# Optimization experiments

Measured on AMD Instinct MI355X. Metric: run time of the kernel, lower is better.

The kernel has to match this reference:

```python
import jax, jax.numpy as jnp
import numpy as np


def layer_norm(x, w, b, eps=1e-5):
    mu = jnp.mean(x, axis=-1, keepdims=True)
    var = jnp.mean(jnp.square(x - mu), axis=-1, keepdims=True)
    return (x - mu) / jnp.sqrt(var + eps) * w + b


def setup_inputs() -> dict:
    B, T, S, D, K = 8, 2048, 2048, 512, 3
    ks = jax.random.split(jax.random.key(0), 8)
    w_scale = 0.02  # modest init so softmax/layernorm stay in a sane range
    return {
        "x": jax.random.normal(ks[0], (B, T, D), jnp.float32),
        "enc": jax.random.normal(ks[1], (B, S, D), jnp.float32),
        "conv_w": jax.random.normal(ks[2], (2 * D, D, K), jnp.float32) * w_scale,
        "conv_b": jnp.zeros((2 * D,), jnp.float32),
        "ln1_w": jnp.ones((D,), jnp.float32),
        "ln1_b": jnp.zeros((D,), jnp.float32),
        "Wq": jax.random.normal(ks[3], (D, D), jnp.float32) * w_scale,
        "bq": jnp.zeros((D,), jnp.float32),
        "Wk": jax.random.normal(ks[4], (D, D), jnp.float32) * w_scale,
        "bk": jnp.zeros((D,), jnp.float32),
        "Wv": jax.random.normal(ks[5], (D, D), jnp.float32) * w_scale,
        "bv": jnp.zeros((D,), jnp.float32),
        "Wo": jax.random.normal(ks[6], (D, D), jnp.float32) * w_scale,
        "bo": jnp.zeros((D,), jnp.float32),
        "ln2_w": jnp.ones((D,), jnp.float32),
        "ln2_b": jnp.zeros((D,), jnp.float32),
    }


def reference(x, enc, conv_w, conv_b, ln1_w, ln1_b, Wq, bq, Wk, bk, Wv, bv, Wo, bo, ln2_w, ln2_b):
    D = x.shape[-1]
    K = conv_w.shape[-1]
    # Causal GLU: left-pad by K-1 so each output sees only past/current positions.
    xt = jnp.transpose(x, (0, 2, 1))  # [B, D, T]
    xt = jnp.pad(xt, ((0, 0), (0, 0), (K - 1, 0)))
    conv = jax.lax.conv_general_dilated(
        xt, conv_w, window_strides=(1,), padding="VALID",
        dimension_numbers=("NCH", "OIH", "NCH"))
    conv = conv + conv_b[None, :, None]
    conv = jnp.transpose(conv, (0, 2, 1))  # [B, T, 2D]
    a, g = jnp.split(conv, 2, axis=-1)
    glu = a * jax.nn.sigmoid(g)
    # residual + LN1 (dropout is identity in eval mode)
    h = layer_norm(glu + x, ln1_w, ln1_b)
    # cross-attention: bmm -> softmax -> bmm (single head)
    q = h @ Wq.T + bq            # [B, T, D]
    k = enc @ Wk.T + bk          # [B, S, D]
    v = enc @ Wv.T + bv          # [B, S, D]
    scores = jnp.einsum("btd,bsd->bts", q, k) / jnp.sqrt(jnp.float32(D))
    attn = jax.nn.softmax(scores, axis=-1)  # [B, T, S]
    ctx = jnp.einsum("bts,bsd->btd", attn, v)
    ctx = ctx @ Wo.T + bo
    out = layer_norm(h + ctx, ln2_w, ln2_b)
    return out, attn
```

## Files before the change

### kernel.cpp

```cpp
#include <hip/hip_runtime.h>
#include <hip/hip_bf16.h>
#include <stdint.h>


typedef unsigned short ushortT;
typedef __bf16 bf16x8 __attribute__((ext_vector_type(8)));
typedef float floatx4 __attribute__((ext_vector_type(4)));
typedef unsigned short ushort4v __attribute__((ext_vector_type(4)));
typedef unsigned short ushort8 __attribute__((ext_vector_type(8)));

__device__ __forceinline__ ushortT f2bf(float f) {
  unsigned u = __builtin_bit_cast(unsigned, f);
  u += 0x7FFFu + ((u >> 16) & 1u);
  return (ushortT)(u >> 16);
}
__device__ __forceinline__ float bf2f(ushortT u) {
  return __builtin_bit_cast(float, (unsigned)u << 16);
}

__device__ __forceinline__ void gload_lds16(const void* g, void* l) {
  __builtin_amdgcn_global_load_lds(
      (const __attribute__((address_space(1))) void*)g,
      (__attribute__((address_space(3))) void*)l, 16, 0, 0);
}

__global__ __launch_bounds__(256)
void k_f32_to_bf16v(const float* __restrict__ src, ushortT* __restrict__ dst, long n4) {
  long i = (long)blockIdx.x * 256 + threadIdx.x;
  if (i >= n4) return;
  floatx4 v = *(const floatx4*)&src[i * 4];
  ushort4v o;
#pragma unroll
  for (int j = 0; j < 4; j++) o[j] = f2bf(v[j]);
  *(ushort4v*)&dst[i * 4] = o;
}

__global__ __launch_bounds__(256)
void k_w4(const float* __restrict__ w0, const float* __restrict__ w1,
          const float* __restrict__ w2, const float* __restrict__ w3,
          ushortT* __restrict__ dst) {
  long i = (long)blockIdx.x * 256 + threadIdx.x;
  int m = (int)(i >> 16);
  long within = (i & 65535) * 4;
  const float* s = (m == 0) ? w0 : (m == 1) ? w1 : (m == 2) ? w2 : w3;
  floatx4 v = *(const floatx4*)&s[within];
  ushort4v o;
#pragma unroll
  for (int j = 0; j < 4; j++) o[j] = f2bf(v[j]);
  *(ushort4v*)&dst[(long)m * 262144 + within] = o;
}

__global__ __launch_bounds__(128)
void k_xpad(const float* __restrict__ x, ushortT* __restrict__ xp) {
  int row = blockIdx.x;
  int b = row / 2050, tp = row % 2050;
  int c = threadIdx.x * 4;
  ushort4v o = {0, 0, 0, 0};
  if (tp >= 2) {
    floatx4 v = *(const floatx4*)&x[((long)(b * 2048 + tp - 2)) * 512 + c];
#pragma unroll
    for (int j = 0; j < 4; j++) o[j] = f2bf(v[j]);
  }
  *(ushort4v*)&xp[(long)row * 512 + c] = o;
}

__global__ __launch_bounds__(256)
void k_convw(const float* __restrict__ w, ushortT* __restrict__ dst) {
  long idx = (long)blockIdx.x * 256 + threadIdx.x;
  if (idx >= 1024L * 1536) return;
  int n = (int)(idx / 1536), kk = (int)(idx % 1536);
  int tap = kk >> 9, i = kk & 511;
  int o = ((n >> 4) & 1) * 512 + (n >> 5) * 16 + (n & 15);
  dst[idx] = f2bf(w[(o * 512 + i) * 3 + tap]);
}

template<int CONV_A, int GLU, int BIAS, int WBF16, int DUALZ, int SWAP>
__global__ __launch_bounds__(512)
void k_gemm256(const ushortT* __restrict__ A, const ushortT* __restrict__ A2, int lda, long aBatch,
               const ushortT* __restrict__ Bm, const ushortT* __restrict__ Bm2, int ldb, long bBatch,
               const float* __restrict__ bias, const float* __restrict__ bias2,
               const float* __restrict__ xres,
               float* __restrict__ Cf, ushortT* __restrict__ Cb, ushortT* __restrict__ Cb2,
               long cBatch, int ldc, int Kdim, float scale)
{
  __shared__ ushortT lds[2][2 * 16384];

  const int tid  = threadIdx.x;
  const int lane = tid & 63;
  const int wave = tid >> 6;
  const int wr   = wave >> 2;
  const int wc   = wave & 3;
  const int l15  = lane & 15;
  const int quad = lane >> 4;

  const ushortT* Ap = A;
  const ushortT* Bp = Bm;
  const float* biasP = bias;
  ushortT* CbP = Cb;
  if (DUALZ && blockIdx.z) { Ap = A2; Bp = Bm2; biasP = bias2; CbP = Cb2; }
  const long zA = DUALZ ? 0 : (long)blockIdx.z * aBatch;
  const long zB = DUALZ ? 0 : (long)blockIdx.z * bBatch;
  const long zC = DUALZ ? 0 : (long)blockIdx.z * cBatch;
  const int rowBase = (SWAP ? blockIdx.y : blockIdx.x) * 256;
  const int colBase = (SWAP ? blockIdx.x : blockIdx.y) * 256;

  auto STAGE = [&](int t) {
    ushortT* sA = lds[t & 1];
    ushortT* sB = sA + 16384;
    const int k0 = t << 6;
#pragma unroll
    for (int l = 0; l < 4; l++) {
      int idx = l * 512 + tid;
      int row = idx >> 3;
      int ck  = ((tid & 7) ^ (row & 7)) << 3;
      if (CONV_A) {
        int gr = rowBase + row;
        int gc = k0 + ck;
        int tap = gc >> 9, ii = gc & 511;
        int b = gr >> 11, tt = gr & 2047;
        long gofs = ((long)(b * 2050 + tt + tap) << 9) + ii;
        gload_lds16(Ap + gofs, sA + idx * 8);
      } else {
        long gofs = zA + (long)(rowBase + row) * lda + (k0 + ck);
        gload_lds16(Ap + gofs, sA + idx * 8);
      }
    }
#pragma unroll
    for (int l = 0; l < 4; l++) {
      int idx = l * 512 + tid;
      int row = idx >> 3;
      int ck  = ((tid & 7) ^ (row & 7)) << 3;
      long gofs = zB + (long)(colBase + row) * ldb + (k0 + ck);
      gload_lds16(Bp + gofs, sB + idx * 8);
    }
  };

  auto LD = [&](const ushortT* s, int r, int c) -> bf16x8 {
    return *(const bf16x8*)&s[r * 64 + ((c ^ (r & 7)) << 3)];
  };

  floatx4 zero = {0.f, 0.f, 0.f, 0.f};
  floatx4 acc[8][4];
#pragma unroll
  for (int mi = 0; mi < 8; mi++)
#pragma unroll
    for (int ni = 0; ni < 4; ni++) acc[mi][ni] = zero;

  const int NT = Kdim >> 6;
  STAGE(0);
  STAGE(1);

  for (int t = 0; t < NT; t++) {
    if (t < NT - 1) asm volatile("s_waitcnt vmcnt(8)" ::: "memory");
    else            asm volatile("s_waitcnt vmcnt(0)" ::: "memory");
    __builtin_amdgcn_s_barrier();

    const ushortT* sA = lds[t & 1];
    const ushortT* sB = sA + 16384;

    bf16x8 av[4][2], bv[4][2];
#pragma unroll
    for (int ni = 0; ni < 4; ni++)
#pragma unroll
      for (int ks = 0; ks < 2; ks++)
        bv[ni][ks] = LD(sB, wc * 64 + ni * 16 + l15, ks * 4 + quad);
#pragma unroll
    for (int mi = 0; mi < 4; mi++)
#pragma unroll
      for (int ks = 0; ks < 2; ks++)
        av[mi][ks] = LD(sA, wr * 128 + mi * 16 + l15, ks * 4 + quad);

    __builtin_amdgcn_s_setprio(1);
#pragma unroll
    for (int mi = 0; mi < 4; mi++)
#pragma unroll
      for (int ni = 0; ni < 4; ni++)
#pragma unroll
        for (int ks = 0; ks < 2; ks++)
          acc[mi][ni] = __builtin_amdgcn_mfma_f32_16x16x32_bf16(av[mi][ks], bv[ni][ks], acc[mi][ni], 0, 0, 0);
    __builtin_amdgcn_s_setprio(0);

#pragma unroll
    for (int mi = 0; mi < 4; mi++)
#pragma unroll
      for (int ks = 0; ks < 2; ks++)
        av[mi][ks] = LD(sA, wr * 128 + 64 + mi * 16 + l15, ks * 4 + quad);

    __builtin_amdgcn_s_setprio(1);
#pragma unroll
    for (int mi = 0; mi < 4; mi++)
#pragma unroll
      for (int ni = 0; ni < 4; ni++)
#pragma unroll
        for (int ks = 0; ks < 2; ks++)
          acc[4 + mi][ni] = __builtin_amdgcn_mfma_f32_16x16x32_bf16(av[mi][ks], bv[ni][ks], acc[4 + mi][ni], 0, 0, 0);
    __builtin_amdgcn_s_setprio(0);

    __builtin_amdgcn_s_barrier();
    if (t + 2 < NT) STAGE(t + 2);
  }

  if (GLU) {
#pragma unroll
    for (int mi = 0; mi < 8; mi++) {
#pragma unroll
      for (int ni = 0; ni < 4; ni += 2) {
        int colA = colBase + wc * 64 + ni * 16;
        int d = (colA >> 5) * 16 + l15;
        float ba = biasP[d], bg = biasP[512 + d];
#pragma unroll
        for (int r = 0; r < 4; r++) {
          int grow = rowBase + wr * 128 + mi * 16 + quad * 4 + r;
          float a = acc[mi][ni][r] + ba;
          float g = acc[mi][ni + 1][r] + bg;
          float val = a / (1.0f + __expf(-g)) + xres[(long)grow * 512 + d];
          Cf[(long)grow * 512 + d] = val;
        }
      }
    }
  } else {
#pragma unroll
    for (int mi = 0; mi < 8; mi++) {
#pragma unroll
      for (int ni = 0; ni < 4; ni++) {
        int gcol = colBase + wc * 64 + ni * 16 + l15;
        float bcol = BIAS ? biasP[gcol] : 0.0f;
#pragma unroll
        for (int r = 0; r < 4; r++) {
          int grow = rowBase + wr * 128 + mi * 16 + quad * 4 + r;
          float val = acc[mi][ni][r] * scale + bcol;
          long off = zC + (long)grow * ldc + gcol;
          if (WBF16) CbP[off] = f2bf(val);
          else       Cf[off] = val;
        }
      }
    }
  }
}

template<int BIAS, int WBF16, int LNEPI>
__global__ __launch_bounds__(512)
void k_gemm64(const ushortT* __restrict__ A, int lda, long aBatch,
              const ushortT* __restrict__ Bm, int ldb, long bBatch,
              const float* __restrict__ bias, const ushortT* __restrict__ hres,
              const float* __restrict__ lnw, const float* __restrict__ lnb,
              float* __restrict__ Cf, ushortT* __restrict__ Cb,
              long cBatch, int ldc, int Kdim, float scale)
{
  __shared__ ushortT lds[2][(64 + 512) * 64];

  const int tid  = threadIdx.x;
  const int lane = tid & 63;
  const int wave = tid >> 6;
  const int l15  = lane & 15;
  const int quad = lane >> 4;

  const long zA = (long)blockIdx.z * aBatch;
  const long zB = (long)blockIdx.z * bBatch;
  const long zC = (long)blockIdx.z * cBatch;
  const int rowBase = blockIdx.y * 64;
  const int colBase = blockIdx.x * 512;

  auto STAGE = [&](int t) {
    ushortT* sA = lds[t & 1];
    ushortT* sB = sA + 64 * 64;
    const int k0 = t << 6;
    {
      int row = tid >> 3;
      int ck  = ((tid & 7) ^ (row & 7)) << 3;
      long gofs = zA + (long)(rowBase + row) * lda + (k0 + ck);
      gload_lds16(A + gofs, sA + tid * 8);
    }
#pragma unroll
    for (int l = 0; l < 8; l++) {
      int idx = l * 512 + tid;
      int row = idx >> 3;
      int ck  = ((tid & 7) ^ (row & 7)) << 3;
      long gofs = zB + (long)(colBase + row) * ldb + (k0 + ck);
      gload_lds16(Bm + gofs, sB + idx * 8);
    }
  };

  auto LD = [&](const ushortT* s, int r, int c) -> bf16x8 {
    return *(const bf16x8*)&s[r * 64 + ((c ^ (r & 7)) << 3)];
  };

  floatx4 zero = {0.f, 0.f, 0.f, 0.f};
  floatx4 acc[4][4];
#pragma unroll
  for (int mi = 0; mi < 4; mi++)
#pragma unroll
    for (int ni = 0; ni < 4; ni++) acc[mi][ni] = zero;

  const int NT = Kdim >> 6;
  STAGE(0);
  STAGE(1);

  for (int t = 0; t < NT; t++) {
    if (t < NT - 1) asm volatile("s_waitcnt vmcnt(9)" ::: "memory");
    else            asm volatile("s_waitcnt vmcnt(0)" ::: "memory");
    __builtin_amdgcn_s_barrier();

    const ushortT* sA = lds[t & 1];
    const ushortT* sB = sA + 64 * 64;

    bf16x8 av[4][2], bv[4][2];
#pragma unroll
    for (int ni = 0; ni < 4; ni++)
#pragma unroll
      for (int ks = 0; ks < 2; ks++)
        bv[ni][ks] = LD(sB, wave * 64 + ni * 16 + l15, ks * 4 + quad);
#pragma unroll
    for (int mi = 0; mi < 4; mi++)
#pragma unroll
      for (int ks = 0; ks < 2; ks++)
        av[mi][ks] = LD(sA, mi * 16 + l15, ks * 4 + quad);

    __builtin_amdgcn_s_setprio(1);
#pragma unroll
    for (int mi = 0; mi < 4; mi++)
#pragma unroll
      for (int ni = 0; ni < 4; ni++)
#pragma unroll
        for (int ks = 0; ks < 2; ks++)
          acc[mi][ni] = __builtin_amdgcn_mfma_f32_16x16x32_bf16(av[mi][ks], bv[ni][ks], acc[mi][ni], 0, 0, 0);
    __builtin_amdgcn_s_setprio(0);

    __builtin_amdgcn_s_barrier();
    if (t + 2 < NT) STAGE(t + 2);
  }

  if (LNEPI) {
    float bov[4], lw[4], lb[4];
#pragma unroll
    for (int ni = 0; ni < 4; ni++) {
      int col = wave * 64 + ni * 16 + l15;
      bov[ni] = bias[col]; lw[ni] = lnw[col]; lb[ni] = lnb[col];
    }
    float* psum = (float*)&lds[0][0];
    float* pssq = psum + 8 * 64;
    __syncthreads();
#pragma unroll
    for (int mi = 0; mi < 4; mi++) {
#pragma unroll
      for (int r = 0; r < 4; r++) {
        int rowl = mi * 16 + quad * 4 + r;
        long grow = rowBase + rowl;
        float ps = 0.f, pq = 0.f;
#pragma unroll
        for (int ni = 0; ni < 4; ni++) {
          int col = wave * 64 + ni * 16 + l15;
          float val = acc[mi][ni][r] + bov[ni] + bf2f(hres[grow * 512 + col]);
          acc[mi][ni][r] = val;
          ps += val; pq += val * val;
        }
#pragma unroll
        for (int off = 1; off < 16; off <<= 1) { ps += __shfl_xor(ps, off); pq += __shfl_xor(pq, off); }
        if (l15 == 0) { psum[wave * 64 + rowl] = ps; pssq[wave * 64 + rowl] = pq; }
      }
    }
    __syncthreads();
#pragma unroll
    for (int mi = 0; mi < 4; mi++) {
#pragma unroll
      for (int r = 0; r < 4; r++) {
        int rowl = mi * 16 + quad * 4 + r;
        float S = 0.f, Q = 0.f;
#pragma unroll
        for (int w = 0; w < 8; w++) { S += psum[w * 64 + rowl]; Q += pssq[w * 64 + rowl]; }
        float mu = S * (1.0f / 512.0f);
        float rstd = rsqrtf(Q * (1.0f / 512.0f) - mu * mu + 1e-5f);
        long grow = rowBase + rowl;
#pragma unroll
        for (int ni = 0; ni < 4; ni++) {
          int col = wave * 64 + ni * 16 + l15;
          Cf[grow * 512 + col] = (acc[mi][ni][r] - mu) * rstd * lw[ni] + lb[ni];
        }
      }
    }
  } else {
#pragma unroll
    for (int mi = 0; mi < 4; mi++) {
#pragma unroll
      for (int ni = 0; ni < 4; ni++) {
        int gcol = colBase + wave * 64 + ni * 16 + l15;
        float bcol = (BIAS == 1) ? bias[gcol] : 0.0f;
#pragma unroll
        for (int r = 0; r < 4; r++) {
          int grow = rowBase + mi * 16 + quad * 4 + r;
          float val = acc[mi][ni][r] * scale + bcol + ((BIAS == 2) ? bias[grow] : 0.0f);
          long off = zC + (long)grow * ldc + gcol;
          if (WBF16) Cb[off] = f2bf(val);
          else       Cf[off] = val;
        }
      }
    }
  }
}

__global__ __launch_bounds__(128)
void k_ln(const float* __restrict__ src, const float* __restrict__ w, const float* __restrict__ b,
          ushortT* __restrict__ outb)
{
  __shared__ float s1[2], s2[2];
  long r = blockIdx.x;
  int tid = threadIdx.x;
  floatx4 v = *(const floatx4*)&src[r * 512 + tid * 4];
  float sum = v[0] + v[1] + v[2] + v[3];
  float ssq = v[0]*v[0] + v[1]*v[1] + v[2]*v[2] + v[3]*v[3];
#pragma unroll
  for (int off = 32; off; off >>= 1) { sum += __shfl_xor(sum, off); ssq += __shfl_xor(ssq, off); }
  if ((tid & 63) == 0) { s1[tid >> 6] = sum; s2[tid >> 6] = ssq; }
  __syncthreads();
  sum = s1[0] + s1[1]; ssq = s2[0] + s2[1];
  float mu = sum * (1.0f / 512.0f);
  float var = ssq * (1.0f / 512.0f) - mu * mu;
  float rstd = rsqrtf(var + 1e-5f);
  floatx4 wv = *(const floatx4*)&w[tid * 4];
  floatx4 bv = *(const floatx4*)&b[tid * 4];
  ushort4v ob;
#pragma unroll
  for (int j = 0; j < 4; j++) ob[j] = f2bf((v[j] - mu) * rstd * wv[j] + bv[j]);
  *(ushort4v*)&outb[r * 512 + tid * 4] = ob;
}

__global__ __launch_bounds__(256)
void k_softmax(ushortT* __restrict__ logits, float* __restrict__ attn)
{
  __shared__ float sred[4];
  long r = blockIdx.x;
  ushortT* lrow = logits + r * 2048;
  float* arow = attn + r * 2048;
  int tid = threadIdx.x;
  ushort8 uv = *(const ushort8*)&lrow[tid * 8];
  float v[8];
#pragma unroll
  for (int j = 0; j < 8; j++) v[j] = bf2f(uv[j]);
  float mx = v[0];
#pragma unroll
  for (int j = 1; j < 8; j++) mx = fmaxf(mx, v[j]);
#pragma unroll
  for (int off = 32; off; off >>= 1) mx = fmaxf(mx, __shfl_xor(mx, off));
  if ((tid & 63) == 0) sred[tid >> 6] = mx;
  __syncthreads();
  mx = fmaxf(fmaxf(sred[0], sred[1]), fmaxf(sred[2], sred[3]));
  __syncthreads();
  float sum = 0.f;
#pragma unroll
  for (int j = 0; j < 8; j++) { v[j] = __expf(v[j] - mx); sum += v[j]; }
#pragma unroll
  for (int off = 32; off; off >>= 1) sum += __shfl_xor(sum, off);
  if ((tid & 63) == 0) sred[tid >> 6] = sum;
  __syncthreads();
  sum = sred[0] + sred[1] + sred[2] + sred[3];
  float inv = 1.0f / sum;
  floatx4 o0, o1;
  ushort8 ob;
#pragma unroll
  for (int j = 0; j < 8; j++) {
    float p = v[j] * inv;
    if (j < 4) o0[j] = p; else o1[j - 4] = p;
    ob[j] = f2bf(p);
  }
  *(floatx4*)&arow[tid * 8] = o0;
  *(floatx4*)&arow[tid * 8 + 4] = o1;
  *(ushort8*)&lrow[tid * 8] = ob;
}

extern "C" void kernel_launch(void* const* d_in, const int* in_sizes, int n_in,
                              void* d_out, int out_size, void* d_ws, size_t ws_size,
                              hipStream_t stream)
{
  const float* x      = (const float*)d_in[0];
  const float* enc    = (const float*)d_in[1];
  const float* conv_w = (const float*)d_in[2];
  const float* conv_b = (const float*)d_in[3];
  const float* ln1_w  = (const float*)d_in[4];
  const float* ln1_b  = (const float*)d_in[5];
  const float* Wq     = (const float*)d_in[6];
  const float* bq     = (const float*)d_in[7];
  const float* Wk     = (const float*)d_in[8];
  const float* bk     = (const float*)d_in[9];
  const float* Wv     = (const float*)d_in[10];
  const float* bv     = (const float*)d_in[11];
  const float* Wo     = (const float*)d_in[12];
  const float* bo     = (const float*)d_in[13];
  const float* ln2_w  = (const float*)d_in[14];
  const float* ln2_b  = (const float*)d_in[15];

  const long BT = 16384, Dd = 512, S = 2048, TT = 2048;
  float* out  = (float*)d_out;
  float* attn = out + BT * Dd;

  char* p = (char*)d_ws;
  auto alloc = [&](size_t bytes) { char* r = p; p += (bytes + 255) & ~255UL; return r; };
  float*   hglu  = (float*)alloc(BT * Dd * 4);
  ushortT* xpad  = (ushortT*)alloc(8L * 2050 * 512 * 2);
  ushortT* encbf = (ushortT*)alloc(BT * Dd * 2);
  ushortT* hbf   = (ushortT*)alloc(BT * Dd * 2);
  ushortT* qbf   = (ushortT*)alloc(BT * Dd * 2);
  ushortT* kbf   = (ushortT*)alloc(BT * Dd * 2);
  ushortT* vT    = (ushortT*)alloc(Dd * BT * 2);
  ushortT* ctxbf = (ushortT*)alloc(BT * Dd * 2);
  ushortT* sl    = (ushortT*)alloc(BT * S * 2);
  ushortT* Wcbf  = (ushortT*)alloc(1024L * 1536 * 2);
  ushortT* wall  = (ushortT*)alloc(4L * 262144 * 2);
  ushortT* Wqbf = wall, *Wkbf = wall + 262144, *Wvbf = wall + 2 * 262144, *Wobf = wall + 3 * 262144;

  k_xpad<<<8 * 2050, 128, 0, stream>>>(x, xpad);
  k_f32_to_bf16v<<<(BT * Dd / 4 + 255) / 256, 256, 0, stream>>>(enc, encbf, BT * Dd / 4);
  k_convw<<<(1024 * 1536 + 255) / 256, 256, 0, stream>>>(conv_w, Wcbf);
  k_w4<<<1024, 256, 0, stream>>>(Wq, Wk, Wv, Wo, wall);

  k_gemm256<1, 1, 0, 0, 0, 0><<<dim3(64, 4, 1), 512, 0, stream>>>(
      xpad, nullptr, 0, 0, Wcbf, nullptr, 1536, 0,
      conv_b, nullptr, x, hglu, nullptr, nullptr, 0, 512, 1536, 1.0f);
  k_ln<<<16384, 128, 0, stream>>>(hglu, ln1_w, ln1_b, hbf);

  k_gemm256<0, 0, 1, 1, 1, 0><<<dim3(64, 2, 2), 512, 0, stream>>>(
      hbf, encbf, 512, 0, Wqbf, Wkbf, 512, 0,
      bq, bk, nullptr, nullptr, qbf, kbf, 0, 512, 512, 1.0f);

  k_gemm64<2, 1, 0><<<dim3(32, 8, 1), 512, 0, stream>>>(
      Wvbf, 512, 0, encbf, 512, 0,
      bv, nullptr, nullptr, nullptr,
      nullptr, vT, 0, 16384, 512, 1.0f);

  k_gemm256<0, 0, 0, 1, 0, 0><<<dim3(8, 8, 8), 512, 0, stream>>>(
      qbf, nullptr, 512, TT * Dd, kbf, nullptr, 512, S * Dd,
      nullptr, nullptr, nullptr, nullptr, sl, nullptr,
      TT * S, 2048, 512, 0.04419417382415922f);
  k_softmax<<<16384, 256, 0, stream>>>(sl, attn);

  k_gemm64<0, 1, 0><<<dim3(1, 32, 8), 512, 0, stream>>>(
      sl, 2048, TT * S, vT, 16384, TT,
      nullptr, nullptr, nullptr, nullptr,
      nullptr, ctxbf, TT * Dd, 512, 2048, 1.0f);

  k_gemm64<0, 0, 1><<<dim3(1, 256, 1), 512, 0, stream>>>(
      ctxbf, 512, 0, Wobf, 512, 0,
      bo, hbf, ln2_w, ln2_b,
      out, nullptr, 0, 512, 512, 1.0f);
}
```

Measured before the change: 531.2 us.

## Fuse softmax into attention-context GEMM and interleave 256-tile GEMM staging loads

Removes the standalone softmax kernel. A new kernel first computes each row's max and sum from the bf16 logits, then normalizes the probabilities on the fly while staging them into LDS for the P·V GEMM, writing the fp32 attn output along the way. This drops a full read-modify-write pass over the bf16 logits and one launch. The logits are now read twice for the row statistics plus once more for the GEMM. Separately, the 256-tile GEMM splits its prefetch into B and A halves and issues them between the two MFMA phases, with an extra barrier, to overlap loads with compute.

```diff
diff --git a/kernel.cpp b/kernel.cpp
--- a/kernel.cpp
+++ b/kernel.cpp
@@ -104,35 +104,32 @@
   const int rowBase = (SWAP ? blockIdx.y : blockIdx.x) * 256;
   const int colBase = (SWAP ? blockIdx.x : blockIdx.y) * 256;
 
-  auto STAGE = [&](int t) {
+  auto STAGE_A = [&](int t, int l) {
     ushortT* sA = lds[t & 1];
-    ushortT* sB = sA + 16384;
     const int k0 = t << 6;
-#pragma unroll
-    for (int l = 0; l < 4; l++) {
-      int idx = l * 512 + tid;
-      int row = idx >> 3;
-      int ck  = ((tid & 7) ^ (row & 7)) << 3;
-      if (CONV_A) {
-        int gr = rowBase + row;
-        int gc = k0 + ck;
-        int tap = gc >> 9, ii = gc & 511;
-        int b = gr >> 11, tt = gr & 2047;
-        long gofs = ((long)(b * 2050 + tt + tap) << 9) + ii;
-        gload_lds16(Ap + gofs, sA + idx * 8);
-      } else {
-        long gofs = zA + (long)(rowBase + row) * lda + (k0 + ck);
-        gload_lds16(Ap + gofs, sA + idx * 8);
-      }
-    }
-#pragma unroll
-    for (int l = 0; l < 4; l++) {
-      int idx = l * 512 + tid;
-      int row = idx >> 3;
-      int ck  = ((tid & 7) ^ (row & 7)) << 3;
-      long gofs = zB + (long)(colBase + row) * ldb + (k0 + ck);
-      gload_lds16(Bp + gofs, sB + idx * 8);
-    }
+    int idx = l * 512 + tid;
+    int row = idx >> 3;
+    int ck  = ((tid & 7) ^ (row & 7)) << 3;
+    if (CONV_A) {
+      int gr = rowBase + row;
+      int gc = k0 + ck;
+      int tap = gc >> 9, ii = gc & 511;
+      int b = gr >> 11, tt = gr & 2047;
+      long gofs = ((long)(b * 2050 + tt + tap) << 9) + ii;
+      gload_lds16(Ap + gofs, sA + idx * 8);
+    } else {
+      long gofs = zA + (long)(rowBase + row) * lda + (k0 + ck);
+      gload_lds16(Ap + gofs, sA + idx * 8);
+    }
+  };
+  auto STAGE_B = [&](int t, int l) {
+    ushortT* sB = lds[t & 1] + 16384;
+    const int k0 = t << 6;
+    int idx = l * 512 + tid;
+    int row = idx >> 3;
+    int ck  = ((tid & 7) ^ (row & 7)) << 3;
+    long gofs = zB + (long)(colBase + row) * ldb + (k0 + ck);
+    gload_lds16(Bp + gofs, sB + idx * 8);
   };
 
   auto LD = [&](const ushortT* s, int r, int c) -> bf16x8 {
@@ -147,8 +144,14 @@
     for (int ni = 0; ni < 4; ni++) acc[mi][ni] = zero;
 
   const int NT = Kdim >> 6;
-  STAGE(0);
-  STAGE(1);
+#pragma unroll
+  for (int l = 0; l < 4; l++) { STAGE_B(0, l); }
+#pragma unroll
+  for (int l = 0; l < 4; l++) { STAGE_A(0, l); }
+#pragma unroll
+  for (int l = 0; l < 4; l++) { STAGE_B(1, l); }
+#pragma unroll
+  for (int l = 0; l < 4; l++) { STAGE_A(1, l); }
 
   for (int t = 0; t < NT; t++) {
     if (t < NT - 1) asm volatile("s_waitcnt vmcnt(8)" ::: "memory");
@@ -180,11 +183,18 @@
           acc[mi][ni] = __builtin_amdgcn_mfma_f32_16x16x32_bf16(av[mi][ks], bv[ni][ks], acc[mi][ni], 0, 0, 0);
     __builtin_amdgcn_s_setprio(0);
 
+    __builtin_amdgcn_s_barrier();
+
 #pragma unroll
     for (int mi = 0; mi < 4; mi++)
 #pragma unroll
       for (int ks = 0; ks < 2; ks++)
         av[mi][ks] = LD(sA, wr * 128 + 64 + mi * 16 + l15, ks * 4 + quad);
+
+    if (t + 2 < NT) {
+      STAGE_B(t + 2, 0); STAGE_B(t + 2, 1); STAGE_B(t + 2, 2); STAGE_B(t + 2, 3);
+      STAGE_A(t + 2, 0); STAGE_A(t + 2, 2);
+    }
 
     __builtin_amdgcn_s_setprio(1);
 #pragma unroll
@@ -197,7 +207,7 @@
     __builtin_amdgcn_s_setprio(0);
 
     __builtin_amdgcn_s_barrier();
-    if (t + 2 < NT) STAGE(t + 2);
+    if (t + 2 < NT) { STAGE_A(t + 2, 1); STAGE_A(t + 2, 3); }
   }
 
   if (GLU) {
@@ -398,6 +408,150 @@
   }
 }
 
+__global__ __launch_bounds__(512)
+void k_ctx_sm(const ushortT* __restrict__ logit,
+              const ushortT* __restrict__ vT,
+              float* __restrict__ attn,
+              ushortT* __restrict__ ctxb)
+{
+  __shared__ ushortT sB[2][512 * 64];
+  __shared__ ushortT sA[2][64 * 64];
+  __shared__ float rowM[64], rowInv[64];
+
+  const int tid = threadIdx.x, lane = tid & 63, wave = tid >> 6;
+  const int l15 = lane & 15, quad = lane >> 4;
+  const int z = blockIdx.z;
+  const int rowBase = blockIdx.y * 64;
+  const long lrowBase = (long)z * 2048 + rowBase;
+
+  {
+    int r = tid >> 3, c0 = (tid & 7) * 256;
+    const ushortT* lp = logit + (lrowBase + r) * 2048 + c0;
+    float m = -3.0e38f;
+    for (int i = 0; i < 32; i++) {
+      ushort8 u = *(const ushort8*)&lp[i * 8];
+#pragma unroll
+      for (int j = 0; j < 8; j++) m = fmaxf(m, bf2f(u[j]));
+    }
+    m = fmaxf(m, __shfl_xor(m, 1));
+    m = fmaxf(m, __shfl_xor(m, 2));
+    m = fmaxf(m, __shfl_xor(m, 4));
+    float s = 0.f;
+    for (int i = 0; i < 32; i++) {
+      ushort8 u = *(const ushort8*)&lp[i * 8];
+#pragma unroll
+      for (int j = 0; j < 8; j++) s += __expf(bf2f(u[j]) - m);
+    }
+    s += __shfl_xor(s, 1);
+    s += __shfl_xor(s, 2);
+    s += __shfl_xor(s, 4);
+    if ((tid & 7) == 0) { rowM[r] = m; rowInv[r] = 1.0f / s; }
+  }
+  __syncthreads();
+
+  const int rA = tid >> 3, cA = tid & 7;
+  const float Mr = rowM[rA], Ir = rowInv[rA];
+
+  auto STAGEB = [&](int t) {
+    ushortT* d = sB[t & 1];
+    const int k0 = t << 6;
+#pragma unroll
+    for (int l = 0; l < 8; l++) {
+      int idx = l * 512 + tid;
+      int row = idx >> 3;
+      int ck = ((tid & 7) ^ (row & 7)) << 3;
+      long gofs = (long)row * 16384 + (long)z * 2048 + k0 + ck;
+      gload_lds16(vT + gofs, d + idx * 8);
+    }
+  };
+  auto ALOAD = [&](int t) -> ushort8 {
+    return *(const ushort8*)&logit[(lrowBase + rA) * 2048 + (t << 6) + cA * 8];
+  };
+  auto APUT = [&](int t, ushort8 u) {
+    floatx4 p0, p1;
+    ushort8 pb;
+#pragma unroll
+    for (int j = 0; j < 8; j++) {
+      float p = __expf(bf2f(u[j]) - Mr) * Ir;
+      if (j < 4) p0[j] = p; else p1[j - 4] = p;
+      pb[j] = f2bf(p);
+    }
+    float* ap = attn + (lrowBase + rA) * 2048 + (t << 6) + cA * 8;
+    *(floatx4*)ap = p0;
+    *(floatx4*)(ap + 4) = p1;
+    *(ushort8*)&sA[t & 1][rA * 64 + ((cA ^ (rA & 7)) << 3)] = pb;
+  };
+  auto LD = [&](const ushortT* s, int r, int c) -> bf16x8 {
+    return *(const bf16x8*)&s[r * 64 + ((c ^ (r & 7)) << 3)];
+  };
+
+  floatx4 zero = {0.f, 0.f, 0.f, 0.f};
+  floatx4 acc[4][4];
+#pragma unroll
+  for (int mi = 0; mi < 4; mi++)
+#pragma unroll
+    for (int ni = 0; ni < 4; ni++) acc[mi][ni] = zero;
+
+  const int NT = 32;
+  ushort8 aCur = ALOAD(0); STAGEB(0);
+  ushort8 aNxt = ALOAD(1); STAGEB(1);
+  APUT(0, aCur);
+  asm volatile("s_waitcnt vmcnt(9)" ::: "memory");
+  asm volatile("s_waitcnt lgkmcnt(0)" ::: "memory");
+  __builtin_amdgcn_s_barrier();
+
+  ushort8 aNew = aNxt;
+  for (int t = 0; t < NT; t++) {
+    const ushortT* cA_ = sA[t & 1];
+    const ushortT* cB_ = sB[t & 1];
+    bf16x8 av[4][2], bv[4][2];
+#pragma unroll
+    for (int ni = 0; ni < 4; ni++)
+#pragma unroll
+      for (int ks = 0; ks < 2; ks++)
+        bv[ni][ks] = LD(cB_, wave * 64 + ni * 16 + l15, ks * 4 + quad);
+#pragma unroll
+    for (int mi = 0; mi < 4; mi++)
+#pragma unroll
+      for (int ks = 0; ks < 2; ks++)
+        av[mi][ks] = LD(cA_, mi * 16 + l15, ks * 4 + quad);
+
+    __builtin_amdgcn_s_setprio(1);
+#pragma unroll
+    for (int mi = 0; mi < 4; mi++)
+#pragma unroll
+      for (int ni = 0; ni < 4; ni++)
+#pragma unroll
+        for (int ks = 0; ks < 2; ks++)
+          acc[mi][ni] = __builtin_amdgcn_mfma_f32_16x16x32_bf16(av[mi][ks], bv[ni][ks], acc[mi][ni], 0, 0, 0);
+    __builtin_amdgcn_s_setprio(0);
+
+    __builtin_amdgcn_s_barrier();
+    if (t + 2 < NT) { aNew = ALOAD(t + 2); STAGEB(t + 2); }
+    if (t + 1 < NT) {
+      if (t + 2 < NT) asm volatile("s_waitcnt vmcnt(9)" ::: "memory");
+      else            asm volatile("s_waitcnt vmcnt(0)" ::: "memory");
+      APUT(t + 1, aNxt);
+      aNxt = aNew;
+      asm volatile("s_waitcnt lgkmcnt(0)" ::: "memory");
+    }
+    __builtin_amdgcn_s_barrier();
+  }
+
+#pragma unroll
+  for (int mi = 0; mi < 4; mi++) {
+#pragma unroll
+    for (int ni = 0; ni < 4; ni++) {
+      int col = wave * 64 + ni * 16 + l15;
+#pragma unroll
+      for (int r = 0; r < 4; r++) {
+        long grow = lrowBase + mi * 16 + quad * 4 + r;
+        ctxb[grow * 512 + col] = f2bf(acc[mi][ni][r]);
+      }
+    }
+  }
+}
+
 __global__ __launch_bounds__(128)
 void k_ln(const float* __restrict__ src, const float* __restrict__ w, const float* __restrict__ b,
           ushortT* __restrict__ outb)
@@ -422,49 +576,6 @@
 #pragma unroll
   for (int j = 0; j < 4; j++) ob[j] = f2bf((v[j] - mu) * rstd * wv[j] + bv[j]);
   *(ushort4v*)&outb[r * 512 + tid * 4] = ob;
-}
-
-__global__ __launch_bounds__(256)
-void k_softmax(ushortT* __restrict__ logits, float* __restrict__ attn)
-{
-  __shared__ float sred[4];
-  long r = blockIdx.x;
-  ushortT* lrow = logits + r * 2048;
-  float* arow = attn + r * 2048;
-  int tid = threadIdx.x;
-  ushort8 uv = *(const ushort8*)&lrow[tid * 8];
-  float v[8];
-#pragma unroll
-  for (int j = 0; j < 8; j++) v[j] = bf2f(uv[j]);
-  float mx = v[0];
-#pragma unroll
-  for (int j = 1; j < 8; j++) mx = fmaxf(mx, v[j]);
-#pragma unroll
-  for (int off = 32; off; off >>= 1) mx = fmaxf(mx, __shfl_xor(mx, off));
-  if ((tid & 63) == 0) sred[tid >> 6] = mx;
-  __syncthreads();
-  mx = fmaxf(fmaxf(sred[0], sred[1]), fmaxf(sred[2], sred[3]));
-  __syncthreads();
-  float sum = 0.f;
-#pragma unroll
-  for (int j = 0; j < 8; j++) { v[j] = __expf(v[j] - mx); sum += v[j]; }
-#pragma unroll
-  for (int off = 32; off; off >>= 1) sum += __shfl_xor(sum, off);
-  if ((tid & 63) == 0) sred[tid >> 6] = sum;
-  __syncthreads();
-  sum = sred[0] + sred[1] + sred[2] + sred[3];
-  float inv = 1.0f / sum;
-  floatx4 o0, o1;
-  ushort8 ob;
-#pragma unroll
-  for (int j = 0; j < 8; j++) {
-    float p = v[j] * inv;
-    if (j < 4) o0[j] = p; else o1[j - 4] = p;
-    ob[j] = f2bf(p);
-  }
-  *(floatx4*)&arow[tid * 8] = o0;
-  *(floatx4*)&arow[tid * 8 + 4] = o1;
-  *(ushort8*)&lrow[tid * 8] = ob;
 }
 
 extern "C" void kernel_launch(void* const* d_in, const int* in_sizes, int n_in,
@@ -530,12 +641,8 @@
       qbf, nullptr, 512, TT * Dd, kbf, nullptr, 512, S * Dd,
       nullptr, nullptr, nullptr, nullptr, sl, nullptr,
       TT * S, 2048, 512, 0.04419417382415922f);
-  k_softmax<<<16384, 256, 0, stream>>>(sl, attn);
-
-  k_gemm64<0, 1, 0><<<dim3(1, 32, 8), 512, 0, stream>>>(
-      sl, 2048, TT * S, vT, 16384, TT,
-      nullptr, nullptr, nullptr, nullptr,
-      nullptr, ctxbf, TT * Dd, 512, 2048, 1.0f);
+
+  k_ctx_sm<<<dim3(1, 32, 8), 512, 0, stream>>>(sl, vT, attn, ctxbf);
 
   k_gemm64<0, 0, 1><<<dim3(1, 256, 1), 512, 0, stream>>>(
       ctxbf, 512, 0, Wobf, 512, 0,
```

Result: no change. 538.9 us (+1.5%).

## Interleave next-tile loads into GEMM compute and retile the attention-context GEMM

Applied to the files above, without the earlier changes.

The 256x256 GEMM now splits tile staging into per-slice A and B loads. Part of the next-next tile's loads (all of B and half of A) is issued between the two MFMA halves, once an extra barrier guarantees the overwritten LDS regions are no longer being read. This overlaps global-to-LDS traffic with matrix-core work instead of bunching it at the end of the iteration. The attn·V product also moves from the generic 64-row kernel to a dedicated 128x256-tile kernel with batch-interleaved block indices, which changes per-block reuse and the work split. The trade-offs are an extra barrier per iteration and a fragile ordering between LDS reads and async writes into the same buffer.

```diff
diff --git a/kernel.cpp b/kernel.cpp
--- a/kernel.cpp
+++ b/kernel.cpp
@@ -104,35 +104,32 @@
   const int rowBase = (SWAP ? blockIdx.y : blockIdx.x) * 256;
   const int colBase = (SWAP ? blockIdx.x : blockIdx.y) * 256;
 
-  auto STAGE = [&](int t) {
+  auto STAGE_A = [&](int t, int l) {
     ushortT* sA = lds[t & 1];
-    ushortT* sB = sA + 16384;
     const int k0 = t << 6;
-#pragma unroll
-    for (int l = 0; l < 4; l++) {
-      int idx = l * 512 + tid;
-      int row = idx >> 3;
-      int ck  = ((tid & 7) ^ (row & 7)) << 3;
-      if (CONV_A) {
-        int gr = rowBase + row;
-        int gc = k0 + ck;
-        int tap = gc >> 9, ii = gc & 511;
-        int b = gr >> 11, tt = gr & 2047;
-        long gofs = ((long)(b * 2050 + tt + tap) << 9) + ii;
-        gload_lds16(Ap + gofs, sA + idx * 8);
-      } else {
-        long gofs = zA + (long)(rowBase + row) * lda + (k0 + ck);
-        gload_lds16(Ap + gofs, sA + idx * 8);
-      }
-    }
-#pragma unroll
-    for (int l = 0; l < 4; l++) {
-      int idx = l * 512 + tid;
-      int row = idx >> 3;
-      int ck  = ((tid & 7) ^ (row & 7)) << 3;
-      long gofs = zB + (long)(colBase + row) * ldb + (k0 + ck);
-      gload_lds16(Bp + gofs, sB + idx * 8);
-    }
+    int idx = l * 512 + tid;
+    int row = idx >> 3;
+    int ck  = ((tid & 7) ^ (row & 7)) << 3;
+    if (CONV_A) {
+      int gr = rowBase + row;
+      int gc = k0 + ck;
+      int tap = gc >> 9, ii = gc & 511;
+      int b = gr >> 11, tt = gr & 2047;
+      long gofs = ((long)(b * 2050 + tt + tap) << 9) + ii;
+      gload_lds16(Ap + gofs, sA + idx * 8);
+    } else {
+      long gofs = zA + (long)(rowBase + row) * lda + (k0 + ck);
+      gload_lds16(Ap + gofs, sA + idx * 8);
+    }
+  };
+  auto STAGE_B = [&](int t, int l) {
+    ushortT* sB = lds[t & 1] + 16384;
+    const int k0 = t << 6;
+    int idx = l * 512 + tid;
+    int row = idx >> 3;
+    int ck  = ((tid & 7) ^ (row & 7)) << 3;
+    long gofs = zB + (long)(colBase + row) * ldb + (k0 + ck);
+    gload_lds16(Bp + gofs, sB + idx * 8);
   };
 
   auto LD = [&](const ushortT* s, int r, int c) -> bf16x8 {
@@ -147,8 +144,14 @@
     for (int ni = 0; ni < 4; ni++) acc[mi][ni] = zero;
 
   const int NT = Kdim >> 6;
-  STAGE(0);
-  STAGE(1);
+#pragma unroll
+  for (int l = 0; l < 4; l++) { STAGE_B(0, l); }
+#pragma unroll
+  for (int l = 0; l < 4; l++) { STAGE_A(0, l); }
+#pragma unroll
+  for (int l = 0; l < 4; l++) { STAGE_B(1, l); }
+#pragma unroll
+  for (int l = 0; l < 4; l++) { STAGE_A(1, l); }
 
   for (int t = 0; t < NT; t++) {
     if (t < NT - 1) asm volatile("s_waitcnt vmcnt(8)" ::: "memory");
@@ -180,11 +183,18 @@
           acc[mi][ni] = __builtin_amdgcn_mfma_f32_16x16x32_bf16(av[mi][ks], bv[ni][ks], acc[mi][ni], 0, 0, 0);
     __builtin_amdgcn_s_setprio(0);
 
+    __builtin_amdgcn_s_barrier();
+
 #pragma unroll
     for (int mi = 0; mi < 4; mi++)
 #pragma unroll
       for (int ks = 0; ks < 2; ks++)
         av[mi][ks] = LD(sA, wr * 128 + 64 + mi * 16 + l15, ks * 4 + quad);
+
+    if (t + 2 < NT) {
+      STAGE_B(t + 2, 0); STAGE_B(t + 2, 1); STAGE_B(t + 2, 2); STAGE_B(t + 2, 3);
+      STAGE_A(t + 2, 0); STAGE_A(t + 2, 2);
+    }
 
     __builtin_amdgcn_s_setprio(1);
 #pragma unroll
@@ -197,7 +207,7 @@
     __builtin_amdgcn_s_setprio(0);
 
     __builtin_amdgcn_s_barrier();
-    if (t + 2 < NT) STAGE(t + 2);
+    if (t + 2 < NT) { STAGE_A(t + 2, 1); STAGE_A(t + 2, 3); }
   }
 
   if (GLU) {
@@ -233,6 +243,113 @@
           if (WBF16) CbP[off] = f2bf(val);
           else       Cf[off] = val;
         }
+      }
+    }
+  }
+}
+
+__global__ __launch_bounds__(512)
+void k_ctx128(const ushortT* __restrict__ P,
+              const ushortT* __restrict__ vT,
+              ushortT* __restrict__ ctxb)
+{
+  __shared__ ushortT lds[2][(128 + 256) * 64];
+
+  const int tid  = threadIdx.x;
+  const int lane = tid & 63;
+  const int wave = tid >> 6;
+  const int wr   = wave >> 2;
+  const int wc   = wave & 3;
+  const int l15  = lane & 15;
+  const int quad = lane >> 4;
+
+  const int lid = blockIdx.x;
+  const int z   = lid & 7;
+  const int idx = lid >> 3;
+  const int rowBase = (idx >> 1) * 128;
+  const int colBase = (idx & 1) * 256;
+  const long zA = (long)z * 2048 * 2048;
+
+  auto STAGE = [&](int t) {
+    ushortT* sA = lds[t & 1];
+    ushortT* sB = sA + 128 * 64;
+    const int k0 = t << 6;
+#pragma unroll
+    for (int l = 0; l < 2; l++) {
+      int i2 = l * 512 + tid;
+      int row = i2 >> 3;
+      int ck  = ((tid & 7) ^ (row & 7)) << 3;
+      long gofs = zA + (long)(rowBase + row) * 2048 + (k0 + ck);
+      gload_lds16(P + gofs, sA + i2 * 8);
+    }
+#pragma unroll
+    for (int l = 0; l < 4; l++) {
+      int i2 = l * 512 + tid;
+      int row = i2 >> 3;
+      int ck  = ((tid & 7) ^ (row & 7)) << 3;
+      long gofs = (long)(colBase + row) * 16384 + (long)z * 2048 + (k0 + ck);
+      gload_lds16(vT + gofs, sB + i2 * 8);
+    }
+  };
+
+  auto LD = [&](const ushortT* s, int r, int c) -> bf16x8 {
+    return *(const bf16x8*)&s[r * 64 + ((c ^ (r & 7)) << 3)];
+  };
+
+  floatx4 zero = {0.f, 0.f, 0.f, 0.f};
+  floatx4 acc[4][4];
+#pragma unroll
+  for (int mi = 0; mi < 4; mi++)
+#pragma unroll
+    for (int ni = 0; ni < 4; ni++) acc[mi][ni] = zero;
+
+  const int NT = 32;
+  STAGE(0);
+  STAGE(1);
+
+  for (int t = 0; t < NT; t++) {
+    if (t < NT - 1) asm volatile("s_waitcnt vmcnt(6)" ::: "memory");
+    else            asm volatile("s_waitcnt vmcnt(0)" ::: "memory");
+    __builtin_amdgcn_s_barrier();
+
+    const ushortT* sA = lds[t & 1];
+    const ushortT* sB = sA + 128 * 64;
+
+    bf16x8 av[4][2], bv[4][2];
+#pragma unroll
+    for (int ni = 0; ni < 4; ni++)
+#pragma unroll
+      for (int ks = 0; ks < 2; ks++)
+        bv[ni][ks] = LD(sB, wc * 64 + ni * 16 + l15, ks * 4 + quad);
+#pragma unroll
+    for (int mi = 0; mi < 4; mi++)
+#pragma unroll
+      for (int ks = 0; ks < 2; ks++)
+        av[mi][ks] = LD(sA, wr * 64 + mi * 16 + l15, ks * 4 + quad);
+
+    __builtin_amdgcn_s_setprio(1);
+#pragma unroll
+    for (int mi = 0; mi < 4; mi++)
+#pragma unroll
+      for (int ni = 0; ni < 4; ni++)
+#pragma unroll
+        for (int ks = 0; ks < 2; ks++)
+          acc[mi][ni] = __builtin_amdgcn_mfma_f32_16x16x32_bf16(av[mi][ks], bv[ni][ks], acc[mi][ni], 0, 0, 0);
+    __builtin_amdgcn_s_setprio(0);
+
+    __builtin_amdgcn_s_barrier();
+    if (t + 2 < NT) STAGE(t + 2);
+  }
+
+#pragma unroll
+  for (int mi = 0; mi < 4; mi++) {
+#pragma unroll
+    for (int ni = 0; ni < 4; ni++) {
+      int col = colBase + wc * 64 + ni * 16 + l15;
+#pragma unroll
+      for (int r = 0; r < 4; r++) {
+        long grow = (long)z * 2048 + rowBase + wr * 64 + mi * 16 + quad * 4 + r;
+        ctxb[grow * 512 + col] = f2bf(acc[mi][ni][r]);
       }
     }
   }
@@ -532,10 +649,7 @@
       TT * S, 2048, 512, 0.04419417382415922f);
   k_softmax<<<16384, 256, 0, stream>>>(sl, attn);
 
-  k_gemm64<0, 1, 0><<<dim3(1, 32, 8), 512, 0, stream>>>(
-      sl, 2048, TT * S, vT, 16384, TT,
-      nullptr, nullptr, nullptr, nullptr,
-      nullptr, ctxbf, TT * Dd, 512, 2048, 1.0f);
+  k_ctx128<<<256, 512, 0, stream>>>(sl, vT, ctxbf);
 
   k_gemm64<0, 0, 1><<<dim3(1, 256, 1), 512, 0, stream>>>(
       ctxbf, 512, 0, Wobf, 512, 0,
```

Result: faster. 499.4 us (-6.0%).
